# Kernel optimization log

Measured on AMD Instinct MI355X. Metric: run time of the kernel, lower is better.

Reference implementation:

```python
import jax, jax.numpy as jnp
import numpy as np

EPS = 1e-08
SIGMA = 0.1
B = 1.0


def setup_inputs() -> dict:
    key = jax.random.key(0)
    k1, k2 = jax.random.split(key)
    N, C, H, W = 4, 256, 64, 64
    featureT = jax.random.normal(k1, (N, C, H, W), dtype=jnp.float32)
    featureI = jax.random.normal(k2, (N, C, H, W), dtype=jnp.float32)
    return {"featureT": featureT, "featureI": featureI}


def reference(featureT, featureI):
    N, C, H, W = featureT.shape
    # center both by target mean over (batch, spatial)
    meanT = featureT.mean(axis=(0, 2, 3), keepdims=True)
    fI = featureI - meanT
    fT = featureT - meanT
    # channel-wise L2 normalize
    fI = fI / (jnp.linalg.norm(fI, axis=1, keepdims=True) + EPS)
    fT = fT / (jnp.linalg.norm(fT, axis=1, keepdims=True) + EPS)
    # 1x1-patch conv2d == contraction over channels: sim[n, p, h, w]
    # where p indexes the flattened H*W spatial positions of the target.
    fT_flat = fT.reshape(N, C, H * W)  # [N, C, P]
    sim = jnp.einsum('nchw,ncp->nphw', fI, fT_flat)  # [N, P, H, W]
    raw_dist = (1.0 - sim) / 2.0
    # relative distances: divide by min over patch axis
    div = jnp.min(raw_dist, axis=1, keepdims=True)
    relative_dist = raw_dist / (div + EPS)
    # contextual similarity: exp-weight + sum-normalize over patch axis
    Wt = jnp.exp((B - relative_dist) / (SIGMA + EPS))
    W_sum = Wt.sum(axis=1, keepdims=True)
    CX = Wt / (W_sum + EPS)
    # max over spatial dims of featureI, mean over patches, -log, mean over batch
    CX = CX.max(axis=(2, 3))           # [N, P]
    CX = CX.mean(axis=1)               # [N]
    CX_loss = -jnp.log(CX + EPS)
    return jnp.mean(CX_loss)
```

## Files before the change

### kernel.cpp

```cpp
#include <hip/hip_runtime.h>
#include <cmath>


#define NB 4
#define CC 256
#define HW 4096
#define NQ0 8
#define NP1 32

static constexpr float kEPS = 1e-8f;
static constexpr float kSIG = 0.1f + 1e-8f;

typedef __attribute__((ext_vector_type(8)))  short short8;
typedef __attribute__((ext_vector_type(16))) float f32x16;

enum {
  OFF_MEAN = 0,
  OFF_CMAX = 256,
  OFF_WSUM = OFF_CMAX + NQ0*NB*HW,
  OFF_MAXV = OFF_WSUM + NP1*NB*HW,
  OFF_GB   = OFF_MAXV + NB*HW,
  OFF_GT   = OFF_GB + 2*NB*HW,
  OFF_GI   = OFF_GT + NB*HW*CC/2,
  OFF_S    = OFF_GI + NB*HW*CC/2,
  WS_FLOATS_FULL = OFF_S + NB*HW*HW/2
};

__device__ __forceinline__ ushort cvt_bf16(float x) {
  unsigned u = __float_as_uint(x);
  unsigned r = (u + 0x7fffu + ((u >> 16) & 1u)) >> 16;
  return (ushort)r;
}
__device__ __forceinline__ float bf2f(ushort u) {
  return __uint_as_float((unsigned)u << 16);
}

__device__ __forceinline__ float blockSum256(float v) {
  __shared__ float sh[4];
  const int lane = threadIdx.x & 63, wv = threadIdx.x >> 6;
  #pragma unroll
  for (int o = 32; o > 0; o >>= 1) v += __shfl_down(v, o, 64);
  __syncthreads();
  if (lane == 0) sh[wv] = v;
  __syncthreads();
  return sh[0] + sh[1] + sh[2] + sh[3];
}

__global__ __launch_bounds__(256) void k_mean9(const float* __restrict__ fT,
                                               float* __restrict__ ws) {
  const int c = blockIdx.x, t = threadIdx.x;
  float s = 0.f;
  for (int n = 0; n < NB; ++n) {
    const float* p = fT + (size_t)(n*CC + c)*HW;
    #pragma unroll
    for (int k = 0; k < 16; ++k) s += p[k*256 + t];
  }
  const float tot = blockSum256(s);
  if (t == 0) ws[OFF_MEAN + c] = tot * (1.0f/16384.0f);
}

__global__ __launch_bounds__(256) void k_prep9(const float* __restrict__ fT,
                                               const float* __restrict__ fI,
                                               float* __restrict__ ws) {
  __shared__ float stage[32][257];
  __shared__ float prt[8][32];
  __shared__ float sinv[32];
  const int t = threadIdx.x, l = t & 63;
  int bid = blockIdx.x;
  const int tensor = (bid >= 512); bid &= 511;
  const int n   = bid >> 7;
  const int r32 = bid & 127;
  const int p0  = r32 * 32;

  const float* __restrict__ src = tensor ? fI : fT;
  ushort* __restrict__ dst = (ushort*)(ws + (tensor ? OFF_GI : OFF_GT));
  const float* __restrict__ mean = ws + OFF_MEAN;

  const int pl = t & 31, cg = t >> 5;
  float acc = 0.f;
  #pragma unroll
  for (int i = 0; i < 32; ++i) {
    const int c = cg*32 + i;
    const float v = src[((size_t)(n*CC + c))*HW + p0 + pl] - mean[c];
    stage[pl][c] = v;
    acc += v*v;
  }
  prt[cg][pl] = acc;
  __syncthreads();
  if (t < 32) {
    float s = 0.f;
    #pragma unroll
    for (int g = 0; g < 8; ++g) s += prt[g][t];
    sinv[t] = 1.0f/(sqrtf(s) + kEPS);
  }
  __syncthreads();

  const int w = t >> 6, lhi = l >> 5, m = l & 31;
  const float iv = sinv[m];
  #pragma unroll
  for (int i = 0; i < 4; ++i) {
    const int kc = w*4 + i;
    const int cb = kc*16 + lhi*8;
    short8 o;
    #pragma unroll
    for (int j = 0; j < 8; ++j)
      ((ushort*)&o)[j] = cvt_bf16(stage[m][cb + j] * iv);
    *(short8*)(dst + (((size_t)(n*128 + r32)*16 + kc) << 9) + l*8) = o;
  }
}

__global__ __launch_bounds__(256, 4) void k_gemm9(
    const ushort* __restrict__ gA, const ushort* __restrict__ gB,
    float* __restrict__ ws)
{
  __shared__ ushort Ab[2][8192];
  __shared__ float red2[128];

  const int t = threadIdx.x;
  const int w = t >> 6, l = t & 63;
  const int ln31 = l & 31, lhi = l >> 5;

  const int b = blockIdx.x;
  const int h = b & 7, sid = b >> 3;
  const int n = sid >> 5;
  const int col0 = (sid & 31) * 128;

  const ushort* __restrict__ gAn = gA + (size_t)(n*128 + h*16)*8192;

  short8 pf[4];
  #pragma unroll
  for (int i = 0; i < 4; ++i)
    pf[i] = *(const short8*)(gAn + (size_t)(i*256 + t)*8);
  #pragma unroll
  for (int i = 0; i < 4; ++i)
    *(short8*)&Ab[0][(i*256 + t)*8] = pf[i];
  #pragma unroll
  for (int i = 0; i < 4; ++i)
    pf[i] = *(const short8*)(gAn + 8192 + (size_t)(i*256 + t)*8);

  const int RB = (col0 >> 5) + w;
  short8 breg[16];
  #pragma unroll
  for (int kc = 0; kc < 16; ++kc)
    breg[kc] = *(const short8*)(gB +
        (((size_t)(n*128 + RB)*16 + kc) << 9) + l*8);

  const int qc = col0 + w*32 + ln31;
  ushort* __restrict__ Sq = (ushort*)(ws + OFF_S) + (size_t)n*HW*HW + qc;

  float runl = -3.0e38f;

  for (int iter = 0; iter < 16; ++iter) {
    const int p = iter & 1;
    __syncthreads();
    if (iter + 1 < 16) {
      #pragma unroll
      for (int i = 0; i < 4; ++i)
        *(short8*)&Ab[p^1][(i*256 + t)*8] = pf[i];
      if (iter + 2 < 16) {
        const ushort* __restrict__ src = gAn + (size_t)(iter + 2)*8192;
        #pragma unroll
        for (int i = 0; i < 4; ++i)
          pf[i] = *(const short8*)(src + (size_t)(i*256 + t)*8);
      }
    }

    f32x16 acc;
    #pragma unroll
    for (int e = 0; e < 16; ++e) acc[e] = 0.f;
    #pragma unroll
    for (int kc = 0; kc < 16; ++kc) {
      const short8 a0 = *(const short8*)&Ab[p][kc*512 + l*8];
      acc = __builtin_amdgcn_mfma_f32_32x32x16_bf16(a0, breg[kc], acc, 0, 0, 0);
    }

    const int pb = h*512 + iter*32 + 4*lhi;
    #pragma unroll
    for (int r = 0; r < 16; ++r) {
      const int prow = pb + (r & 3) + 8*(r >> 2);
      const ushort u = cvt_bf16(acc[r]);
      Sq[(size_t)prow * HW] = u;
      runl = fmaxf(runl, bf2f(u));
    }
  }

  {
    const float o = __shfl_xor(runl, 32, 64);
    runl = fmaxf(runl, o);
  }
  if (l < 32) red2[w*32 + ln31] = runl;
  __syncthreads();
  if (t < 128)
    ws[OFF_CMAX + h*(NB*HW) + n*HW + col0 + t] = red2[t];
}

__global__ __launch_bounds__(256) void k_pass1(float* __restrict__ ws) {
  const int t = threadIdx.x;
  const int b = blockIdx.x;
  const int pc = b & 31, rest = b >> 5;
  const int n = rest >> 3, qblk = rest & 7;
  const int q = qblk*512 + 2*t;

  float a0, b0, a1, b1;
  {
    float cm0 = -3.0e38f, cm1 = -3.0e38f;
    #pragma unroll
    for (int hh = 0; hh < NQ0; ++hh) {
      cm0 = fmaxf(cm0, ws[OFF_CMAX + hh*(NB*HW) + n*HW + q]);
      cm1 = fmaxf(cm1, ws[OFF_CMAX + hh*(NB*HW) + n*HW + q + 1]);
    }
    const float i0 = 1.0f/(2.0f*(0.5f*(1.0f - cm0) + kEPS));
    const float i1 = 1.0f/(2.0f*(0.5f*(1.0f - cm1) + kEPS));
    b0 = i0 / kSIG; a0 = (1.0f - i0) / kSIG;
    b1 = i1 / kSIG; a1 = (1.0f - i1) / kSIG;
  }

  const ushort* __restrict__ S =
      (const ushort*)(ws + OFF_S) + (size_t)n*HW*HW + q;
  float acc0 = 0.f, acc1 = 0.f;
  const int p0 = pc*128;
  #pragma unroll 8
  for (int i = 0; i < 128; ++i) {
    const ushort2 u = *(const ushort2*)(S + (size_t)(p0 + i)*HW);
    acc0 += __expf(fmaf(b0, bf2f(u.x), a0));
    acc1 += __expf(fmaf(b1, bf2f(u.y), a1));
  }
  float2 o; o.x = acc0; o.y = acc1;
  *(float2*)&ws[OFF_WSUM + pc*(NB*HW) + n*HW + q] = o;
}

__global__ __launch_bounds__(256) void k_gb9(float* __restrict__ ws) {
  const int idx = blockIdx.x*256 + threadIdx.x;
  float cm = -3.0e38f;
  #pragma unroll
  for (int hh = 0; hh < NQ0; ++hh)
    cm = fmaxf(cm, ws[OFF_CMAX + hh*(NB*HW) + idx]);
  const float inv2d = 1.0f/(2.0f*(0.5f*(1.0f - cm) + kEPS));
  const float beta  = inv2d / kSIG;
  const float alpha = (1.0f - inv2d) / kSIG;
  float sw = 0.f;
  #pragma unroll
  for (int pc = 0; pc < NP1; ++pc)
    sw += ws[OFF_WSUM + pc*(NB*HW) + idx];
  ws[OFF_GB + idx]         = alpha - logf(sw + kEPS);
  ws[OFF_GB + NB*HW + idx] = beta;
}

__global__ __launch_bounds__(256) void k_pass2(float* __restrict__ ws) {
  __shared__ float gq[4096], bq[4096];
  const int t = threadIdx.x, w = t >> 6, l = t & 63;
  const int b = blockIdx.x;
  const int n = b >> 8, pg = b & 255;

  const float* __restrict__ G  = ws + OFF_GB + n*HW;
  const float* __restrict__ Bq = ws + OFF_GB + NB*HW + n*HW;
  #pragma unroll
  for (int i = 0; i < 4; ++i) {
    *(float4*)&gq[(i*256 + t)*4] = *(const float4*)&G [(i*256 + t)*4];
    *(float4*)&bq[(i*256 + t)*4] = *(const float4*)&Bq[(i*256 + t)*4];
  }
  __syncthreads();

  const ushort* __restrict__ S =
      (const ushort*)(ws + OFF_S) + (size_t)n*HW*HW;
  #pragma unroll
  for (int r = 0; r < 4; ++r) {
    const int p = pg*16 + w*4 + r;
    const ushort* __restrict__ row = S + (size_t)p*HW;
    float m = -3.0e38f;
    #pragma unroll 4
    for (int it = 0; it < 32; ++it) {
      const int q = it*128 + 2*l;
      const ushort2 u = *(const ushort2*)(row + q);
      m = fmaxf(m, fmaf(bq[q],     bf2f(u.x), gq[q]));
      m = fmaxf(m, fmaf(bq[q + 1], bf2f(u.y), gq[q + 1]));
    }
    #pragma unroll
    for (int o = 32; o > 0; o >>= 1) m = fmaxf(m, __shfl_xor(m, o, 64));
    if (l == 0) ws[OFF_MAXV + n*HW + p] = m;
  }
}

__global__ __launch_bounds__(256) void k_final9(const float* __restrict__ ws,
                                                float* __restrict__ out) {
  const int t = threadIdx.x;
  float loss = 0.f;
  for (int n = 0; n < NB; ++n) {
    float s = 0.f;
    for (int k = 0; k < 16; ++k)
      s += __expf(ws[OFF_MAXV + n*HW + k*256 + t]);
    const float tot = blockSum256(s);
    loss += -logf(tot*(1.0f/4096.0f) + kEPS);
  }
  if (t == 0) out[0] = loss*0.25f;
}

extern "C" void kernel_launch(void* const* d_in, const int* in_sizes, int n_in,
                              void* d_out, int out_size, void* d_ws, size_t ws_size,
                              hipStream_t stream) {
  const float* fT = (const float*)d_in[0];
  const float* fI = (const float*)d_in[1];
  float* out = (float*)d_out;
  float* ws  = (float*)d_ws;

  const size_t need_full = (size_t)WS_FLOATS_FULL * sizeof(float);
  if (ws_size < need_full) return;

  const ushort* GT = (const ushort*)(ws + OFF_GT);
  const ushort* GI = (const ushort*)(ws + OFF_GI);
  k_mean9 <<<256,  256, 0, stream>>>(fT, ws);
  k_prep9 <<<1024, 256, 0, stream>>>(fT, fI, ws);
  k_gemm9 <<<1024, 256, 0, stream>>>(GT, GI, ws);
  k_pass1 <<<1024, 256, 0, stream>>>(ws);
  k_gb9   <<<64,   256, 0, stream>>>(ws);
  k_pass2 <<<1024, 256, 0, stream>>>(ws);
  k_final9<<<1,    256, 0, stream>>>(ws, out);
}
```

Before: 205.1 us.

## Store similarity matrix transposed and restructure softmax-sum and max passes

```diff
diff --git a/kernel.cpp b/kernel.cpp
--- a/kernel.cpp
+++ b/kernel.cpp
@@ -6,7 +6,7 @@
 #define CC 256
 #define HW 4096
 #define NQ0 8
-#define NP1 32
+#define NQH 8
 
 static constexpr float kEPS = 1e-8f;
 static constexpr float kSIG = 0.1f + 1e-8f;
@@ -17,10 +17,9 @@
 enum {
   OFF_MEAN = 0,
   OFF_CMAX = 256,
-  OFF_WSUM = OFF_CMAX + NQ0*NB*HW,
-  OFF_MAXV = OFF_WSUM + NP1*NB*HW,
-  OFF_GB   = OFF_MAXV + NB*HW,
-  OFF_GT   = OFF_GB + 2*NB*HW,
+  OFF_GB   = OFF_CMAX + NQ0*NB*HW,
+  OFF_MAXV = OFF_GB + 2*NB*HW,
+  OFF_GT   = OFF_MAXV + NQH*NB*HW,
   OFF_GI   = OFF_GT + NB*HW*CC/2,
   OFF_S    = OFF_GI + NB*HW*CC/2,
   WS_FLOATS_FULL = OFF_S + NB*HW*HW/2
@@ -46,7 +45,7 @@
   return sh[0] + sh[1] + sh[2] + sh[3];
 }
 
-__global__ __launch_bounds__(256) void k_mean9(const float* __restrict__ fT,
+__global__ __launch_bounds__(256) void k_meanA(const float* __restrict__ fT,
                                                float* __restrict__ ws) {
   const int c = blockIdx.x, t = threadIdx.x;
   float s = 0.f;
@@ -59,7 +58,7 @@
   if (t == 0) ws[OFF_MEAN + c] = tot * (1.0f/16384.0f);
 }
 
-__global__ __launch_bounds__(256) void k_prep9(const float* __restrict__ fT,
+__global__ __launch_bounds__(256) void k_prepA(const float* __restrict__ fT,
                                                const float* __restrict__ fI,
                                                float* __restrict__ ws) {
   __shared__ float stage[32][257];
@@ -109,7 +108,7 @@
   }
 }
 
-__global__ __launch_bounds__(256, 4) void k_gemm9(
+__global__ __launch_bounds__(256, 4) void k_gemmA(
     const ushort* __restrict__ gA, const ushort* __restrict__ gB,
     float* __restrict__ ws)
 {
@@ -146,7 +145,8 @@
         (((size_t)(n*128 + RB)*16 + kc) << 9) + l*8);
 
   const int qc = col0 + w*32 + ln31;
-  ushort* __restrict__ Sq = (ushort*)(ws + OFF_S) + (size_t)n*HW*HW + qc;
+  ushort* __restrict__ Srow =
+      (ushort*)(ws + OFF_S) + (size_t)n*HW*HW + (size_t)qc*HW;
 
   float runl = -3.0e38f;
 
@@ -176,11 +176,15 @@
 
     const int pb = h*512 + iter*32 + 4*lhi;
     #pragma unroll
-    for (int r = 0; r < 16; ++r) {
-      const int prow = pb + (r & 3) + 8*(r >> 2);
-      const ushort u = cvt_bf16(acc[r]);
-      Sq[(size_t)prow * HW] = u;
-      runl = fmaxf(runl, bf2f(u));
+    for (int g = 0; g < 4; ++g) {
+      ushort4 u;
+      u.x = cvt_bf16(acc[g*4 + 0]);
+      u.y = cvt_bf16(acc[g*4 + 1]);
+      u.z = cvt_bf16(acc[g*4 + 2]);
+      u.w = cvt_bf16(acc[g*4 + 3]);
+      *(ushort4*)(Srow + pb + 8*g) = u;
+      runl = fmaxf(runl, fmaxf(fmaxf(bf2f(u.x), bf2f(u.y)),
+                               fmaxf(bf2f(u.z), bf2f(u.w))));
     }
   }
 
@@ -194,101 +198,87 @@
     ws[OFF_CMAX + h*(NB*HW) + n*HW + col0 + t] = red2[t];
 }
 
-__global__ __launch_bounds__(256) void k_pass1(float* __restrict__ ws) {
+__global__ __launch_bounds__(256) void k_pass1A(float* __restrict__ ws) {
+  const int t = threadIdx.x, w = t >> 6, l = t & 63;
+  const int b = blockIdx.x;
+  const int n = b >> 7, qg = b & 127;
+
+  const ushort* __restrict__ S =
+      (const ushort*)(ws + OFF_S) + (size_t)n*HW*HW;
+
+  #pragma unroll
+  for (int rr = 0; rr < 8; ++rr) {
+    const int q = qg*32 + w*8 + rr;
+    float cm = -3.0e38f;
+    #pragma unroll
+    for (int hh = 0; hh < NQ0; ++hh)
+      cm = fmaxf(cm, ws[OFF_CMAX + hh*(NB*HW) + n*HW + q]);
+    const float inv2d = 1.0f/(2.0f*(0.5f*(1.0f - cm) + kEPS));
+    const float beta  = inv2d / kSIG;
+    const float alpha = (1.0f - inv2d) / kSIG;
+
+    const ushort* __restrict__ row = S + (size_t)q*HW;
+    float acc = 0.f;
+    #pragma unroll 4
+    for (int it = 0; it < 16; ++it) {
+      const ushort4 u = *(const ushort4*)(row + it*256 + l*4);
+      acc += __expf(fmaf(beta, bf2f(u.x), alpha));
+      acc += __expf(fmaf(beta, bf2f(u.y), alpha));
+      acc += __expf(fmaf(beta, bf2f(u.z), alpha));
+      acc += __expf(fmaf(beta, bf2f(u.w), alpha));
+    }
+    #pragma unroll
+    for (int o = 32; o > 0; o >>= 1) acc += __shfl_down(acc, o, 64);
+    if (l == 0) {
+      ws[OFF_GB + n*HW + q]         = alpha - logf(acc + kEPS);
+      ws[OFF_GB + NB*HW + n*HW + q] = beta;
+    }
+  }
+}
+
+__global__ __launch_bounds__(256) void k_pass2A(float* __restrict__ ws) {
+  __shared__ float gq[512], bq[512];
   const int t = threadIdx.x;
   const int b = blockIdx.x;
-  const int pc = b & 31, rest = b >> 5;
-  const int n = rest >> 3, qblk = rest & 7;
-  const int q = qblk*512 + 2*t;
-
-  float a0, b0, a1, b1;
-  {
-    float cm0 = -3.0e38f, cm1 = -3.0e38f;
-    #pragma unroll
-    for (int hh = 0; hh < NQ0; ++hh) {
-      cm0 = fmaxf(cm0, ws[OFF_CMAX + hh*(NB*HW) + n*HW + q]);
-      cm1 = fmaxf(cm1, ws[OFF_CMAX + hh*(NB*HW) + n*HW + q + 1]);
-    }
-    const float i0 = 1.0f/(2.0f*(0.5f*(1.0f - cm0) + kEPS));
-    const float i1 = 1.0f/(2.0f*(0.5f*(1.0f - cm1) + kEPS));
-    b0 = i0 / kSIG; a0 = (1.0f - i0) / kSIG;
-    b1 = i1 / kSIG; a1 = (1.0f - i1) / kSIG;
-  }
+  const int qh = b & 7, rest = b >> 3;
+  const int n = rest >> 3, ps = rest & 7;
+
+  #pragma unroll
+  for (int i = 0; i < 2; ++i) {
+    const int r = i*256 + t;
+    gq[r] = ws[OFF_GB + n*HW + qh*512 + r];
+    bq[r] = ws[OFF_GB + NB*HW + n*HW + qh*512 + r];
+  }
+  __syncthreads();
 
   const ushort* __restrict__ S =
-      (const ushort*)(ws + OFF_S) + (size_t)n*HW*HW + q;
-  float acc0 = 0.f, acc1 = 0.f;
-  const int p0 = pc*128;
-  #pragma unroll 8
-  for (int i = 0; i < 128; ++i) {
-    const ushort2 u = *(const ushort2*)(S + (size_t)(p0 + i)*HW);
-    acc0 += __expf(fmaf(b0, bf2f(u.x), a0));
-    acc1 += __expf(fmaf(b1, bf2f(u.y), a1));
-  }
-  float2 o; o.x = acc0; o.y = acc1;
-  *(float2*)&ws[OFF_WSUM + pc*(NB*HW) + n*HW + q] = o;
-}
-
-__global__ __launch_bounds__(256) void k_gb9(float* __restrict__ ws) {
-  const int idx = blockIdx.x*256 + threadIdx.x;
-  float cm = -3.0e38f;
-  #pragma unroll
-  for (int hh = 0; hh < NQ0; ++hh)
-    cm = fmaxf(cm, ws[OFF_CMAX + hh*(NB*HW) + idx]);
-  const float inv2d = 1.0f/(2.0f*(0.5f*(1.0f - cm) + kEPS));
-  const float beta  = inv2d / kSIG;
-  const float alpha = (1.0f - inv2d) / kSIG;
-  float sw = 0.f;
-  #pragma unroll
-  for (int pc = 0; pc < NP1; ++pc)
-    sw += ws[OFF_WSUM + pc*(NB*HW) + idx];
-  ws[OFF_GB + idx]         = alpha - logf(sw + kEPS);
-  ws[OFF_GB + NB*HW + idx] = beta;
-}
-
-__global__ __launch_bounds__(256) void k_pass2(float* __restrict__ ws) {
-  __shared__ float gq[4096], bq[4096];
-  const int t = threadIdx.x, w = t >> 6, l = t & 63;
-  const int b = blockIdx.x;
-  const int n = b >> 8, pg = b & 255;
-
-  const float* __restrict__ G  = ws + OFF_GB + n*HW;
-  const float* __restrict__ Bq = ws + OFF_GB + NB*HW + n*HW;
-  #pragma unroll
-  for (int i = 0; i < 4; ++i) {
-    *(float4*)&gq[(i*256 + t)*4] = *(const float4*)&G [(i*256 + t)*4];
-    *(float4*)&bq[(i*256 + t)*4] = *(const float4*)&Bq[(i*256 + t)*4];
-  }
-  __syncthreads();
-
-  const ushort* __restrict__ S =
-      (const ushort*)(ws + OFF_S) + (size_t)n*HW*HW;
-  #pragma unroll
-  for (int r = 0; r < 4; ++r) {
-    const int p = pg*16 + w*4 + r;
-    const ushort* __restrict__ row = S + (size_t)p*HW;
-    float m = -3.0e38f;
-    #pragma unroll 4
-    for (int it = 0; it < 32; ++it) {
-      const int q = it*128 + 2*l;
-      const ushort2 u = *(const ushort2*)(row + q);
-      m = fmaxf(m, fmaf(bq[q],     bf2f(u.x), gq[q]));
-      m = fmaxf(m, fmaf(bq[q + 1], bf2f(u.y), gq[q + 1]));
-    }
-    #pragma unroll
-    for (int o = 32; o > 0; o >>= 1) m = fmaxf(m, __shfl_xor(m, o, 64));
-    if (l == 0) ws[OFF_MAXV + n*HW + p] = m;
-  }
-}
-
-__global__ __launch_bounds__(256) void k_final9(const float* __restrict__ ws,
+      (const ushort*)(ws + OFF_S) + (size_t)n*HW*HW + (size_t)qh*512*HW
+      + ps*512 + 2*t;
+  float m0 = -3.0e38f, m1 = -3.0e38f;
+  #pragma unroll 4
+  for (int q = 0; q < 512; ++q) {
+    const ushort2 u = *(const ushort2*)(S + (size_t)q*HW);
+    m0 = fmaxf(m0, fmaf(bq[q], bf2f(u.x), gq[q]));
+    m1 = fmaxf(m1, fmaf(bq[q], bf2f(u.y), gq[q]));
+  }
+  float2 o; o.x = m0; o.y = m1;
+  *(float2*)&ws[OFF_MAXV + qh*(NB*HW) + n*HW + ps*512 + 2*t] = o;
+}
+
+__global__ __launch_bounds__(256) void k_finalA(const float* __restrict__ ws,
                                                 float* __restrict__ out) {
   const int t = threadIdx.x;
   float loss = 0.f;
   for (int n = 0; n < NB; ++n) {
     float s = 0.f;
-    for (int k = 0; k < 16; ++k)
-      s += __expf(ws[OFF_MAXV + n*HW + k*256 + t]);
+    for (int k = 0; k < 16; ++k) {
+      const int idx = n*HW + k*256 + t;
+      float mv = ws[OFF_MAXV + idx];
+      #pragma unroll
+      for (int qh = 1; qh < NQH; ++qh)
+        mv = fmaxf(mv, ws[OFF_MAXV + qh*(NB*HW) + idx]);
+      s += __expf(mv);
+    }
     const float tot = blockSum256(s);
     loss += -logf(tot*(1.0f/4096.0f) + kEPS);
   }
@@ -308,11 +298,10 @@
 
   const ushort* GT = (const ushort*)(ws + OFF_GT);
   const ushort* GI = (const ushort*)(ws + OFF_GI);
-  k_mean9 <<<256,  256, 0, stream>>>(fT, ws);
-  k_prep9 <<<1024, 256, 0, stream>>>(fT, fI, ws);
-  k_gemm9 <<<1024, 256, 0, stream>>>(GT, GI, ws);
-  k_pass1 <<<1024, 256, 0, stream>>>(ws);
-  k_gb9   <<<64,   256, 0, stream>>>(ws);
-  k_pass2 <<<1024, 256, 0, stream>>>(ws);
-  k_final9<<<1,    256, 0, stream>>>(ws, out);
-}
+  k_meanA <<<256,  256, 0, stream>>>(fT, ws);
+  k_prepA <<<1024, 256, 0, stream>>>(fT, fI, ws);
+  k_gemmA <<<1024, 256, 0, stream>>>(GT, GI, ws);
+  k_pass1A<<<512,  256, 0, stream>>>(ws);
+  k_pass2A<<<256,  256, 0, stream>>>(ws);
+  k_finalA<<<1,    256, 0, stream>>>(ws, out);
+}
```

Result: slower. 232.0 us (+13.1%).
